# Optimization experiments

Hardware: AMD Instinct MI355X
Metric: run time of the kernel (lower is better)

The kernel has to match this reference:

```python
import jax, jax.numpy as jnp
import numpy as np
from jax.scipy.linalg import expm

ETA = 0.1
B, N = 8192, 64


def setup_inputs() -> dict:
    key = jax.random.key(0)
    k_r, k_g = jax.random.split(key)
    # R must be strictly positive: torch.log is ELEMENTWISE log in the original.
    # Shift uniform away from 0 so log(R) stays well-conditioned.
    R = jax.random.uniform(k_r, (B, N, N), dtype=jnp.float32, minval=0.1, maxval=1.0)
    grad = jax.random.normal(k_g, (B, N, N), dtype=jnp.float32)
    return {"R": R, "grad": grad}


def reference(R, grad):
    # skew-symmetric part of the gradient: G - G^T
    skew_grad = grad - jnp.swapaxes(grad, -1, -2)          # [B, N, N]
    # elementwise log (matches torch.log, NOT a matrix logarithm)
    update = jnp.log(R) - ETA * skew_grad                  # [B, N, N]
    # batched matrix exponential (scaling-and-squaring + Pade)
    new_R = jax.vmap(expm)(update)                         # [B, N, N]
    return new_R
```

## Files before the change

kernel.cpp:

```cpp
#include <hip/hip_runtime.h>
#include <math.h>

#define ETA 0.1f

#define C0 1.0f
#define C1 1.0f
#define C2 0.5f
#define C3 (1.0f/6.0f)
#define C4 (1.0f/24.0f)
#define C5 (1.0f/120.0f)
#define C6 (1.0f/720.0f)
#define C7 (1.0f/5040.0f)
#define C8 (1.0f/40320.0f)
#define C9 (1.0f/362880.0f)

typedef __attribute__((ext_vector_type(8))) short short8;
typedef __attribute__((ext_vector_type(4))) float f32x4;

__device__ __forceinline__ int swzF(int r, int cc) { return r * 64 + 4 * (cc ^ (r & 15)); }

__device__ __forceinline__ int rmI(int r, int c) {
    return r * 64 + 8 * ((c >> 3) ^ (r & 7)) + (c & 7);
}
__device__ __forceinline__ int cmI(int r, int c) {
    return c * 64 + 8 * ((r >> 3) ^ (c & 7)) + (r & 7);
}

__device__ __forceinline__ void splitbf(float x, unsigned short& h, unsigned short& l) {
    unsigned u = __float_as_uint(x);
    unsigned r = u + 0x7FFFu + ((u >> 16) & 1u);
    h = (unsigned short)(r >> 16);
    float d = x - __uint_as_float(r & 0xFFFF0000u);
    l = (unsigned short)(__float_as_uint(d) >> 16);
}
__device__ __forceinline__ float bf2f(unsigned short h) {
    return __uint_as_float(((unsigned)h) << 16);
}

__device__ __forceinline__ void mmstage(
    const unsigned short* Ah, const unsigned short* Al,
    const unsigned short* Bh, const unsigned short* Bl,
    unsigned short* Oh, unsigned short* Ol,
    unsigned short* ORh, unsigned short* ORl,
    const unsigned short* BmH, const unsigned short* BmL,
    float cI, float cB, int wv, int lane)
{
    const int n16 = lane & 15;
    const int q = lane >> 4;
    const int mrow = 16 * wv + n16;

    short8 ah[2], al[2], bh[4][2], bl[4][2];
#pragma unroll
    for (int ks = 0; ks < 2; ++ks) {
        int k0 = 32 * ks + 8 * q;
        int ia = rmI(mrow, k0);
        ah[ks] = *(const short8*)(Ah + ia);
        al[ks] = *(const short8*)(Al + ia);
#pragma unroll
        for (int t4 = 0; t4 < 4; ++t4) {
            int ib = cmI(k0, 16 * t4 + n16);
            bh[t4][ks] = *(const short8*)(Bh + ib);
            bl[t4][ks] = *(const short8*)(Bl + ib);
        }
    }

    f32x4 acc[4] = {{0.f,0.f,0.f,0.f},{0.f,0.f,0.f,0.f},{0.f,0.f,0.f,0.f},{0.f,0.f,0.f,0.f}};
#pragma unroll
    for (int ks = 0; ks < 2; ++ks) {
#pragma unroll
        for (int t4 = 0; t4 < 4; ++t4)
            acc[t4] = __builtin_amdgcn_mfma_f32_16x16x32_bf16(ah[ks], bh[t4][ks], acc[t4], 0, 0, 0);
#pragma unroll
        for (int t4 = 0; t4 < 4; ++t4)
            acc[t4] = __builtin_amdgcn_mfma_f32_16x16x32_bf16(al[ks], bl[t4][ks], acc[t4], 0, 0, 0);
#pragma unroll
        for (int t4 = 0; t4 < 4; ++t4)
            acc[t4] = __builtin_amdgcn_mfma_f32_16x16x32_bf16(ah[ks], bl[t4][ks], acc[t4], 0, 0, 0);
#pragma unroll
        for (int t4 = 0; t4 < 4; ++t4)
            acc[t4] = __builtin_amdgcn_mfma_f32_16x16x32_bf16(al[ks], bh[t4][ks], acc[t4], 0, 0, 0);
    }

    const int rbase = 16 * wv + 4 * q;
    if (BmH) {
#pragma unroll
        for (int t4 = 0; t4 < 4; ++t4) {
            int c = 16 * t4 + n16;
            int ib = cmI(rbase, c);
            const ushort4 hh = *(const ushort4*)(BmH + ib);
            const ushort4 ll = *(const ushort4*)(BmL + ib);
            float bmv[4] = { bf2f(hh.x) + bf2f(ll.x), bf2f(hh.y) + bf2f(ll.y),
                             bf2f(hh.z) + bf2f(ll.z), bf2f(hh.w) + bf2f(ll.w) };
#pragma unroll
            for (int rg = 0; rg < 4; ++rg) {
                float v = acc[t4][rg] + cB * bmv[rg];
                if (rbase + rg == c) v += cI;
                acc[t4][rg] = v;
            }
        }
    }

    __syncthreads();

#pragma unroll
    for (int t4 = 0; t4 < 4; ++t4) {
        int c = 16 * t4 + n16;
        unsigned short h[4], l[4];
#pragma unroll
        for (int rg = 0; rg < 4; ++rg) splitbf(acc[t4][rg], h[rg], l[rg]);
        if (Oh) {
            int io = cmI(rbase, c);
            *(ushort4*)(Oh + io) = make_ushort4(h[0], h[1], h[2], h[3]);
            *(ushort4*)(Ol + io) = make_ushort4(l[0], l[1], l[2], l[3]);
        }
        if (ORh) {
#pragma unroll
            for (int rg = 0; rg < 4; ++rg) {
                int io = rmI(rbase + rg, c);
                ORh[io] = h[rg];
                ORl[io] = l[rg];
            }
        }
    }
    __syncthreads();
}

__global__ __launch_bounds__(256, 2) void meg_expm_kernel(
    const float* __restrict__ Rg, const float* __restrict__ Gg,
    float* __restrict__ out)
{
    __shared__ __align__(16) unsigned short sm[32768];
    unsigned short* cm0h = sm;
    unsigned short* cm0l = sm + 4096;
    unsigned short* cm1h = sm + 8192;
    unsigned short* cm1l = sm + 12288;
    unsigned short* bmch = sm + 16384;
    unsigned short* bmcl = sm + 20480;
    unsigned short* rm0h = sm + 24576;
    unsigned short* rm0l = sm + 28672;
    float* FB0 = (float*)sm;
    float* FB1 = (float*)(sm + 8192);
    float* wmax = (float*)(sm + 16384);

    const int t = threadIdx.x;
    const int wv = t >> 6, lane = t & 63;
    const int tx = t & 15, ty = t >> 4;
    const long long base = (long long)blockIdx.x * 4096;

#pragma unroll
    for (int i = 0; i < 4; ++i) {
        int idx = t + i * 256;
        int r = idx >> 4, cc = idx & 15;
        *(float4*)&FB1[swzF(r, cc)] = ((const float4*)(Gg + base))[idx];
    }
    __syncthreads();

#pragma unroll
    for (int i = 0; i < 4; ++i) {
        int r = 4 * ty + i;
        float4 rv = *(const float4*)&Rg[base + r * 64 + 4 * tx];
        float4 gv = *(const float4*)&FB1[swzF(r, tx)];
        float gt[4];
#pragma unroll
        for (int j = 0; j < 4; ++j)
            gt[j] = FB1[swzF(4 * tx + j, r >> 2) + (r & 3)];
        float4 o;
        o.x = logf(rv.x) - ETA * (gv.x - gt[0]);
        o.y = logf(rv.y) - ETA * (gv.y - gt[1]);
        o.z = logf(rv.z) - ETA * (gv.z - gt[2]);
        o.w = logf(rv.w) - ETA * (gv.w - gt[3]);
        *(float4*)&FB0[swzF(r, tx)] = o;
    }
    __syncthreads();

    {
        int c = 16 * wv + (lane & 15);
        int rq = lane >> 4;
        float cs = 0.f;
#pragma unroll
        for (int rr = 0; rr < 16; ++rr) {
            int r = 16 * rq + rr;
            cs += fabsf(FB0[swzF(r, c >> 2) + (c & 3)]);
        }
        cs += __shfl_xor(cs, 16);
        cs += __shfl_xor(cs, 32);
        cs = fmaxf(cs, __shfl_xor(cs, 8));
        cs = fmaxf(cs, __shfl_xor(cs, 4));
        cs = fmaxf(cs, __shfl_xor(cs, 2));
        cs = fmaxf(cs, __shfl_xor(cs, 1));
        if (lane == 0) wmax[wv] = cs;
    }
    __syncthreads();

    const float nrm = fmaxf(fmaxf(wmax[0], wmax[1]), fmaxf(wmax[2], wmax[3]));
    int s = 0;
    if (nrm > 1.0f) {
        s = (int)ceilf(log2f(nrm));
        if (s > 30) s = 30;
        if (s < 0) s = 0;
    }
    const float scale = exp2f(-(float)s);

    unsigned short abmh[4][4], abml[4][4], t0h[4][4], t0l[4][4];
#pragma unroll
    for (int i = 0; i < 4; ++i) {
        int r = 4 * ty + i;
        float4 a = *(const float4*)&FB0[swzF(r, tx)];
        float av[4] = { a.x, a.y, a.z, a.w };
#pragma unroll
        for (int j = 0; j < 4; ++j) {
            float x = av[j] * scale;
            splitbf(x, abmh[i][j], abml[i][j]);
            float t0 = C9 * x + ((r == 4 * tx + j) ? C8 : 0.f);
            splitbf(t0, t0h[i][j], t0l[i][j]);
        }
    }
    __syncthreads();

#pragma unroll
    for (int i = 0; i < 4; ++i) {
        int r = 4 * ty + i;
        *(ushort4*)(rm0h + rmI(r, 4 * tx)) = make_ushort4(abmh[i][0], abmh[i][1], abmh[i][2], abmh[i][3]);
        *(ushort4*)(rm0l + rmI(r, 4 * tx)) = make_ushort4(abml[i][0], abml[i][1], abml[i][2], abml[i][3]);
#pragma unroll
        for (int j = 0; j < 4; ++j) {
            int c = 4 * tx + j;
            int ic = cmI(r, c);
            bmch[ic] = abmh[i][j];
            bmcl[ic] = abml[i][j];
            cm0h[ic] = t0h[i][j];
            cm0l[ic] = t0l[i][j];
        }
    }
    __syncthreads();

    mmstage(rm0h, rm0l, bmch, bmcl, nullptr, nullptr, rm0h, rm0l,
            nullptr, nullptr, 0.f, 0.f, wv, lane);

    mmstage(rm0h, rm0l, cm0h, cm0l, cm1h, cm1l, nullptr, nullptr, bmch, bmcl, C6, C7, wv, lane);
    mmstage(rm0h, rm0l, cm1h, cm1l, cm0h, cm0l, nullptr, nullptr, bmch, bmcl, C4, C5, wv, lane);
    mmstage(rm0h, rm0l, cm0h, cm0l, cm1h, cm1l, nullptr, nullptr, bmch, bmcl, C2, C3, wv, lane);
    mmstage(rm0h, rm0l, cm1h, cm1l, cm0h, cm0l, bmch, bmcl, bmch, bmcl, C0, C1, wv, lane);

    unsigned short *ccmh = cm0h, *ccml = cm0l, *ocmh = cm1h, *ocml = cm1l;
    unsigned short *crmh = bmch, *crml = bmcl, *ormh = rm0h, *orml = rm0l;
    for (int it = 0; it < s; ++it) {
        bool lastp = (it == s - 1);
        mmstage(crmh, crml, ccmh, ccml, ocmh, ocml,
                lastp ? nullptr : ormh, lastp ? nullptr : orml,
                nullptr, nullptr, 0.f, 0.f, wv, lane);
        unsigned short* tp;
        tp = ccmh; ccmh = ocmh; ocmh = tp;
        tp = ccml; ccml = ocml; ocml = tp;
        tp = crmh; crmh = ormh; ormh = tp;
        tp = crml; crml = orml; orml = tp;
    }

#pragma unroll
    for (int i = 0; i < 4; ++i) {
        int g = i * 256 + t;
        int r = g >> 4, cg = g & 15;
        float ov[4];
#pragma unroll
        for (int j = 0; j < 4; ++j) {
            int c = 4 * cg + j;
            int ic = cmI(r, c);
            ov[j] = bf2f(ccmh[ic]) + bf2f(ccml[ic]);
        }
        float4 o;
        o.x = ov[0]; o.y = ov[1]; o.z = ov[2]; o.w = ov[3];
        ((float4*)(out + base))[g] = o;
    }
}

extern "C" void kernel_launch(void* const* d_in, const int* in_sizes, int n_in,
                              void* d_out, int out_size, void* d_ws, size_t ws_size,
                              hipStream_t stream) {
    const float* R = (const float*)d_in[0];
    const float* G = (const float*)d_in[1];
    float* o = (float*)d_out;
    const int B = in_sizes[0] / (64 * 64);
    meg_expm_kernel<<<dim3(B), dim3(256), 0, stream>>>(R, G, o);
}
```

Measured before the change: 581.3 us.

## Halve LDS footprint with in-place Horner stages and register-held scaled matrix

The scaled matrix A is now kept in registers (bmf) instead of a separate LDS copy, and the Horner and squaring stages write their outputs in place into a single pair of row-major and column-major buffers. That cuts shared memory from 64KB to 32KB per block, and launch bounds are raised to 4 blocks per CU so more batches run concurrently. The first stage now computes A^2 while forming the C9*A + C8*I term inside the epilogue. The in-place writes depend on the __syncthreads between the MFMA reads and the stores. The trade-off is more register pressure (16 extra floats per thread plus cmv) under a tighter launch bound, which could cause spills.

```diff
diff --git a/kernel.cpp b/kernel.cpp
--- a/kernel.cpp
+++ b/kernel.cpp
@@ -42,8 +42,8 @@
     const unsigned short* Bh, const unsigned short* Bl,
     unsigned short* Oh, unsigned short* Ol,
     unsigned short* ORh, unsigned short* ORl,
-    const unsigned short* BmH, const unsigned short* BmL,
-    float cI, float cB, int wv, int lane)
+    const float* bmf, float cI, float cB, bool cmIsT0,
+    int wv, int lane)
 {
     const int n16 = lane & 15;
     const int q = lane >> 4;
@@ -82,38 +82,40 @@
     }
 
     const int rbase = 16 * wv + 4 * q;
-    if (BmH) {
-#pragma unroll
-        for (int t4 = 0; t4 < 4; ++t4) {
-            int c = 16 * t4 + n16;
-            int ib = cmI(rbase, c);
-            const ushort4 hh = *(const ushort4*)(BmH + ib);
-            const ushort4 ll = *(const ushort4*)(BmL + ib);
-            float bmv[4] = { bf2f(hh.x) + bf2f(ll.x), bf2f(hh.y) + bf2f(ll.y),
-                             bf2f(hh.z) + bf2f(ll.z), bf2f(hh.w) + bf2f(ll.w) };
-#pragma unroll
-            for (int rg = 0; rg < 4; ++rg) {
-                float v = acc[t4][rg] + cB * bmv[rg];
-                if (rbase + rg == c) v += cI;
-                acc[t4][rg] = v;
-            }
-        }
-    }
-
-    __syncthreads();
-
+    float cmv[4][4];
 #pragma unroll
     for (int t4 = 0; t4 < 4; ++t4) {
         int c = 16 * t4 + n16;
-        unsigned short h[4], l[4];
-#pragma unroll
-        for (int rg = 0; rg < 4; ++rg) splitbf(acc[t4][rg], h[rg], l[rg]);
-        if (Oh) {
+#pragma unroll
+        for (int rg = 0; rg < 4; ++rg) {
+            float a = acc[t4][rg];
+            if (bmf) {
+                float add = cB * bmf[4 * t4 + rg] + ((rbase + rg) == c ? cI : 0.f);
+                if (cmIsT0) { cmv[t4][rg] = add; }
+                else        { a += add; cmv[t4][rg] = a; acc[t4][rg] = a; }
+            } else {
+                cmv[t4][rg] = a;
+            }
+        }
+    }
+
+    __syncthreads();
+
+#pragma unroll
+    for (int t4 = 0; t4 < 4; ++t4) {
+        int c = 16 * t4 + n16;
+        {
+            unsigned short h[4], l[4];
+#pragma unroll
+            for (int rg = 0; rg < 4; ++rg) splitbf(cmv[t4][rg], h[rg], l[rg]);
             int io = cmI(rbase, c);
             *(ushort4*)(Oh + io) = make_ushort4(h[0], h[1], h[2], h[3]);
             *(ushort4*)(Ol + io) = make_ushort4(l[0], l[1], l[2], l[3]);
         }
         if (ORh) {
+            unsigned short h[4], l[4];
+#pragma unroll
+            for (int rg = 0; rg < 4; ++rg) splitbf(acc[t4][rg], h[rg], l[rg]);
 #pragma unroll
             for (int rg = 0; rg < 4; ++rg) {
                 int io = rmI(rbase + rg, c);
@@ -125,22 +127,18 @@
     __syncthreads();
 }
 
-__global__ __launch_bounds__(256, 2) void meg_expm_kernel(
+__global__ __launch_bounds__(256, 4) void meg_expm_kernel(
     const float* __restrict__ Rg, const float* __restrict__ Gg,
     float* __restrict__ out)
 {
-    __shared__ __align__(16) unsigned short sm[32768];
-    unsigned short* cm0h = sm;
-    unsigned short* cm0l = sm + 4096;
-    unsigned short* cm1h = sm + 8192;
-    unsigned short* cm1l = sm + 12288;
-    unsigned short* bmch = sm + 16384;
-    unsigned short* bmcl = sm + 20480;
-    unsigned short* rm0h = sm + 24576;
-    unsigned short* rm0l = sm + 28672;
-    float* FB0 = (float*)sm;
-    float* FB1 = (float*)(sm + 8192);
-    float* wmax = (float*)(sm + 16384);
+    __shared__ __align__(16) unsigned short sm[16384];
+    unsigned short* rmh = sm;
+    unsigned short* rml = sm + 4096;
+    unsigned short* cmh = sm + 8192;
+    unsigned short* cml = sm + 12288;
+    float* FBG = (float*)sm;
+    float* FBA = (float*)(sm + 8192);
+    float* wmax = (float*)sm;
 
     const int t = threadIdx.x;
     const int wv = t >> 6, lane = t & 63;
@@ -151,7 +149,7 @@
     for (int i = 0; i < 4; ++i) {
         int idx = t + i * 256;
         int r = idx >> 4, cc = idx & 15;
-        *(float4*)&FB1[swzF(r, cc)] = ((const float4*)(Gg + base))[idx];
+        *(float4*)&FBG[swzF(r, cc)] = ((const float4*)(Gg + base))[idx];
     }
     __syncthreads();
 
@@ -159,17 +157,17 @@
     for (int i = 0; i < 4; ++i) {
         int r = 4 * ty + i;
         float4 rv = *(const float4*)&Rg[base + r * 64 + 4 * tx];
-        float4 gv = *(const float4*)&FB1[swzF(r, tx)];
+        float4 gv = *(const float4*)&FBG[swzF(r, tx)];
         float gt[4];
 #pragma unroll
         for (int j = 0; j < 4; ++j)
-            gt[j] = FB1[swzF(4 * tx + j, r >> 2) + (r & 3)];
+            gt[j] = FBG[swzF(4 * tx + j, r >> 2) + (r & 3)];
         float4 o;
         o.x = logf(rv.x) - ETA * (gv.x - gt[0]);
         o.y = logf(rv.y) - ETA * (gv.y - gt[1]);
         o.z = logf(rv.z) - ETA * (gv.z - gt[2]);
         o.w = logf(rv.w) - ETA * (gv.w - gt[3]);
-        *(float4*)&FB0[swzF(r, tx)] = o;
+        *(float4*)&FBA[swzF(r, tx)] = o;
     }
     __syncthreads();
 
@@ -180,7 +178,7 @@
 #pragma unroll
         for (int rr = 0; rr < 16; ++rr) {
             int r = 16 * rq + rr;
-            cs += fabsf(FB0[swzF(r, c >> 2) + (c & 3)]);
+            cs += fabsf(FBA[swzF(r, c >> 2) + (c & 3)]);
         }
         cs += __shfl_xor(cs, 16);
         cs += __shfl_xor(cs, 32);
@@ -201,59 +199,58 @@
     }
     const float scale = exp2f(-(float)s);
 
-    unsigned short abmh[4][4], abml[4][4], t0h[4][4], t0l[4][4];
+    unsigned short abmh[4][4], abml[4][4];
 #pragma unroll
     for (int i = 0; i < 4; ++i) {
         int r = 4 * ty + i;
-        float4 a = *(const float4*)&FB0[swzF(r, tx)];
+        float4 a = *(const float4*)&FBA[swzF(r, tx)];
         float av[4] = { a.x, a.y, a.z, a.w };
 #pragma unroll
+        for (int j = 0; j < 4; ++j)
+            splitbf(av[j] * scale, abmh[i][j], abml[i][j]);
+    }
+    __syncthreads();
+
+#pragma unroll
+    for (int i = 0; i < 4; ++i) {
+        int r = 4 * ty + i;
+        *(ushort4*)(rmh + rmI(r, 4 * tx)) = make_ushort4(abmh[i][0], abmh[i][1], abmh[i][2], abmh[i][3]);
+        *(ushort4*)(rml + rmI(r, 4 * tx)) = make_ushort4(abml[i][0], abml[i][1], abml[i][2], abml[i][3]);
+#pragma unroll
         for (int j = 0; j < 4; ++j) {
-            float x = av[j] * scale;
-            splitbf(x, abmh[i][j], abml[i][j]);
-            float t0 = C9 * x + ((r == 4 * tx + j) ? C8 : 0.f);
-            splitbf(t0, t0h[i][j], t0l[i][j]);
-        }
-    }
-    __syncthreads();
-
-#pragma unroll
-    for (int i = 0; i < 4; ++i) {
-        int r = 4 * ty + i;
-        *(ushort4*)(rm0h + rmI(r, 4 * tx)) = make_ushort4(abmh[i][0], abmh[i][1], abmh[i][2], abmh[i][3]);
-        *(ushort4*)(rm0l + rmI(r, 4 * tx)) = make_ushort4(abml[i][0], abml[i][1], abml[i][2], abml[i][3]);
-#pragma unroll
-        for (int j = 0; j < 4; ++j) {
-            int c = 4 * tx + j;
-            int ic = cmI(r, c);
-            bmch[ic] = abmh[i][j];
-            bmcl[ic] = abml[i][j];
-            cm0h[ic] = t0h[i][j];
-            cm0l[ic] = t0l[i][j];
-        }
-    }
-    __syncthreads();
-
-    mmstage(rm0h, rm0l, bmch, bmcl, nullptr, nullptr, rm0h, rm0l,
-            nullptr, nullptr, 0.f, 0.f, wv, lane);
-
-    mmstage(rm0h, rm0l, cm0h, cm0l, cm1h, cm1l, nullptr, nullptr, bmch, bmcl, C6, C7, wv, lane);
-    mmstage(rm0h, rm0l, cm1h, cm1l, cm0h, cm0l, nullptr, nullptr, bmch, bmcl, C4, C5, wv, lane);
-    mmstage(rm0h, rm0l, cm0h, cm0l, cm1h, cm1l, nullptr, nullptr, bmch, bmcl, C2, C3, wv, lane);
-    mmstage(rm0h, rm0l, cm1h, cm1l, cm0h, cm0l, bmch, bmcl, bmch, bmcl, C0, C1, wv, lane);
-
-    unsigned short *ccmh = cm0h, *ccml = cm0l, *ocmh = cm1h, *ocml = cm1l;
-    unsigned short *crmh = bmch, *crml = bmcl, *ormh = rm0h, *orml = rm0l;
+            int ic = cmI(r, 4 * tx + j);
+            cmh[ic] = abmh[i][j];
+            cml[ic] = abml[i][j];
+        }
+    }
+    __syncthreads();
+
+    const int n16 = lane & 15, q = lane >> 4;
+    const int rbase = 16 * wv + 4 * q;
+    float bmf[16];
+#pragma unroll
+    for (int t4 = 0; t4 < 4; ++t4) {
+        int ib = cmI(rbase, 16 * t4 + n16);
+        ushort4 hh = *(const ushort4*)(cmh + ib);
+        ushort4 ll = *(const ushort4*)(cml + ib);
+        bmf[4 * t4 + 0] = bf2f(hh.x) + bf2f(ll.x);
+        bmf[4 * t4 + 1] = bf2f(hh.y) + bf2f(ll.y);
+        bmf[4 * t4 + 2] = bf2f(hh.z) + bf2f(ll.z);
+        bmf[4 * t4 + 3] = bf2f(hh.w) + bf2f(ll.w);
+    }
+
+    mmstage(rmh, rml, cmh, cml, cmh, cml, rmh, rml, bmf, C8, C9, true,  wv, lane);
+
+    mmstage(rmh, rml, cmh, cml, cmh, cml, nullptr, nullptr, bmf, C6, C7, false, wv, lane);
+    mmstage(rmh, rml, cmh, cml, cmh, cml, nullptr, nullptr, bmf, C4, C5, false, wv, lane);
+    mmstage(rmh, rml, cmh, cml, cmh, cml, nullptr, nullptr, bmf, C2, C3, false, wv, lane);
+    mmstage(rmh, rml, cmh, cml, cmh, cml, rmh, rml, bmf, C0, C1, false, wv, lane);
+
     for (int it = 0; it < s; ++it) {
         bool lastp = (it == s - 1);
-        mmstage(crmh, crml, ccmh, ccml, ocmh, ocml,
-                lastp ? nullptr : ormh, lastp ? nullptr : orml,
-                nullptr, nullptr, 0.f, 0.f, wv, lane);
-        unsigned short* tp;
-        tp = ccmh; ccmh = ocmh; ocmh = tp;
-        tp = ccml; ccml = ocml; ocml = tp;
-        tp = crmh; crmh = ormh; ormh = tp;
-        tp = crml; crml = orml; orml = tp;
+        mmstage(rmh, rml, cmh, cml, cmh, cml,
+                lastp ? nullptr : rmh, lastp ? nullptr : rml,
+                nullptr, 0.f, 0.f, false, wv, lane);
     }
 
 #pragma unroll
@@ -265,7 +262,7 @@
         for (int j = 0; j < 4; ++j) {
             int c = 4 * cg + j;
             int ic = cmI(r, c);
-            ov[j] = bf2f(ccmh[ic]) + bf2f(ccml[ic]);
+            ov[j] = bf2f(cmh[ic]) + bf2f(cml[ic]);
         }
         float4 o;
         o.x = ov[0]; o.y = ov[1]; o.z = ov[2]; o.w = ov[3];
```

Measured after the change: 466.6 us. 1.25x faster.
